# Kernel tuning notes

Hardware: AMD Instinct MI355X
Metric: run time of the kernel (lower is better)

The kernel has to match this reference:

```python
import jax, jax.numpy as jnp
import numpy as np

THRESH = 0.2  # contact probability threshold from _make_graph default


def setup_inputs() -> dict:
    key = jax.random.key(0)
    ks = jax.random.split(key, 10)
    L, D, K, M = 1024, 640, 32, 64
    S = jax.random.normal(ks[0], (L, D), jnp.float32)
    P = jax.random.uniform(ks[1], (L, L), jnp.float32)
    P = 0.5 * (P + P.T)  # symmetric base-pair probability matrix
    xyz = jax.random.normal(ks[2], (L, 3), jnp.float32) * 10.0  # Angstrom-scale C1' coords
    rbf_mu = jnp.linspace(0.0, 30.0, K).astype(jnp.float32)     # RBF centers over 0-30 A
    rbf_sigma = jax.random.uniform(ks[3], (K,), jnp.float32, 0.5, 2.0)
    W_edge = jax.random.normal(ks[4], (K + 2, M), jnp.float32) * 0.05
    b_edge = jnp.zeros((M,), jnp.float32)
    W_node = jax.random.normal(ks[5], (D, M), jnp.float32) * 0.05
    w_out = jax.random.normal(ks[6], (M,), jnp.float32) * 0.1
    return {"S": S, "P": P, "xyz": xyz, "rbf_mu": rbf_mu, "rbf_sigma": rbf_sigma,
            "W_edge": W_edge, "b_edge": b_edge, "W_node": W_node, "w_out": w_out}


def reference(S, P, xyz, rbf_mu, rbf_sigma, W_edge, b_edge, W_node, w_out):
    """Graph construction (_make_graph) + one SE3-style gated coordinate update.

    Edges: backbone (j == i+1, etype=0, pij=1) and high-prob contacts
    (P[i,j] > THRESH, j > i+2, etype=1, pij=P[i,j]). Edge scalars are
    [etype, pij, rbf(d)] exactly as in _make_graph; edge vectors are
    xyz[j]-xyz[i]. Computed in dense masked form for jit-compatibility.
    """
    L = xyz.shape[0]
    rel = xyz[None, :, :] - xyz[:, None, :]                      # (L,L,3) xyz[j]-xyz[i]
    # safe norm: eps avoids nan grad on zero diagonal (diagonal is masked out anyway)
    d = jnp.sqrt(jnp.sum(rel * rel, axis=-1, keepdims=True) + 1e-12)  # (L,L,1)
    rbf_feat = jnp.exp(-(d - rbf_mu) ** 2 / (2.0 * rbf_sigma ** 2))   # (L,L,K)

    idx = jnp.arange(L)
    backbone = idx[None, :] == idx[:, None] + 1                  # j == i+1
    contact = (P > THRESH) & (idx[None, :] > idx[:, None] + 2)   # skip j <= i+2
    mask = backbone | contact                                    # (L,L)

    etype = contact.astype(S.dtype)                              # 0 backbone, 1 contact
    pij = jnp.where(backbone, jnp.asarray(1.0, S.dtype), P)
    e_scalar = jnp.concatenate([etype[..., None], pij[..., None], rbf_feat], axis=-1)  # (L,L,K+2)

    # gather-compute: message from edge scalars + destination-node scalars
    node_proj = S @ W_node                                       # (L,M)
    msg = jax.nn.relu(jnp.einsum('ijk,km->ijm', e_scalar, W_edge) + b_edge
                      + node_proj[None, :, :])                   # (L,L,M)
    gate = jax.nn.sigmoid(msg @ w_out) * mask.astype(S.dtype)    # (L,L)

    # scatter: equivariant coordinate update, sum of gated edge vectors per node
    xyz_out = xyz + jnp.einsum('ij,ijc->ic', gate, rel)          # (L,3)
    return xyz_out
```

## Files before the change

### kernel.cpp

```cpp
#include <hip/hip_runtime.h>
#include <math.h>

#define LL 1024
#define DD 640
#define KK 32
#define MM 64
#define THRESH 0.2f
#define LOG2E 1.4426950408889634f

#define NPROJ_OFF  0
#define NPROJC_OFF (NPROJ_OFF + LL * MM)
#define WRT_OFF    (NPROJC_OFF + LL * MM)
#define W1_OFF     (WRT_OFF + 1024)
#define EA_OFF     (W1_OFF + MM)
#define EB_OFF     (EA_OFF + KK)
#define EC_OFF     (EB_OFF + KK)
#define XYZ4_OFF   (EC_OFF + KK)

typedef float f32x4_t __attribute__((ext_vector_type(4)));
typedef short bf16x8_t __attribute__((ext_vector_type(8)));

union FragU { unsigned int u[4]; bf16x8_t v; };

#if __has_builtin(__builtin_amdgcn_sqrtf)
#define FSQRT __builtin_amdgcn_sqrtf
#else
#define FSQRT sqrtf
#endif

#if __has_builtin(__builtin_amdgcn_exp2f)
#define EXP2F __builtin_amdgcn_exp2f
#else
#define EXP2F(x) __expf((x) * 0.6931471805599453f)
#endif

__device__ __forceinline__ unsigned int pack_bf(float hi, float lo) {
    return __builtin_amdgcn_perm(__float_as_uint(hi), __float_as_uint(lo), 0x07060302u);
}

__global__ __launch_bounds__(256) void prep_sk(
    const float* __restrict__ S, const float* __restrict__ xyz,
    const float* __restrict__ rbf_mu, const float* __restrict__ rbf_sigma,
    const float* __restrict__ W_edge, const float* __restrict__ b_edge,
    const float* __restrict__ W_node, float* __restrict__ ws)
{
    const int b = blockIdx.x;
    const int t = threadIdx.x;
    if (b < 256) {
        __shared__ float red[4][64][4];
        const int lane = t & 63;
        const int wave = t >> 6;
        const int r0   = (b >> 2) * 16;
        const int n0   = (b & 3) * 16;
        const int col  = lane & 15;
        const int quad = lane >> 4;

        f32x4_t acc = {0.f, 0.f, 0.f, 0.f};
        const float* arow = S + (size_t)(r0 + col) * DD + wave * 160 + quad * 8;
        const float* bcol = W_node + (size_t)(wave * 160 + quad * 8) * MM + n0 + col;

        #pragma unroll
        for (int ks = 0; ks < 5; ++ks) {
            const float4 a0 = *(const float4*)(arow + ks * 32);
            const float4 a1 = *(const float4*)(arow + ks * 32 + 4);
            FragU A;
            A.u[0] = pack_bf(a0.y, a0.x); A.u[1] = pack_bf(a0.w, a0.z);
            A.u[2] = pack_bf(a1.y, a1.x); A.u[3] = pack_bf(a1.w, a1.z);
            const float* bk = bcol + (size_t)ks * 32 * MM;
            const float b0 = bk[0 * MM], b1 = bk[1 * MM], b2 = bk[2 * MM], b3 = bk[3 * MM];
            const float b4 = bk[4 * MM], b5 = bk[5 * MM], b6 = bk[6 * MM], b7 = bk[7 * MM];
            FragU B;
            B.u[0] = pack_bf(b1, b0); B.u[1] = pack_bf(b3, b2);
            B.u[2] = pack_bf(b5, b4); B.u[3] = pack_bf(b7, b6);
            acc = __builtin_amdgcn_mfma_f32_16x16x32_bf16(A.v, B.v, acc, 0, 0, 0);
        }
        red[wave][lane][0] = acc[0];
        red[wave][lane][1] = acc[1];
        red[wave][lane][2] = acc[2];
        red[wave][lane][3] = acc[3];
        __syncthreads();
        const int lr  = t & 63;
        const int reg = t >> 6;
        const float v = (red[0][lr][reg] + red[1][lr][reg])
                      + (red[2][lr][reg] + red[3][lr][reg]);
        const int row = r0 + (lr >> 4) * 4 + reg;
        const int cc  = n0 + (lr & 15);
        const float vb = v + b_edge[cc];
        ws[NPROJ_OFF  + (size_t)row * MM + cc] = vb;
        ws[NPROJC_OFF + (size_t)row * MM + cc] = vb + W_edge[cc];
    } else {
        unsigned short* wrt = (unsigned short*)(ws + WRT_OFF);
        if (t < MM) ws[W1_OFF + t] = W_edge[MM + t];
        if (t < KK) {
            const float s  = rbf_sigma[t];
            const float m_ = rbf_mu[t];
            const float inv = 1.0f / (2.0f * s * s);
            ws[EA_OFF + t] = -LOG2E * inv;
            ws[EB_OFF + t] =  2.0f * LOG2E * inv * m_;
            ws[EC_OFF + t] = -LOG2E * inv * m_ * m_;
        }
        for (int idx = t; idx < KK * MM; idx += 256) {
            const int m = idx >> 5, k = idx & 31;
            unsigned int u = __float_as_uint(W_edge[(2 + k) * MM + m]);
            u = (u + 0x7fffu + ((u >> 16) & 1u)) >> 16;
            wrt[idx] = (unsigned short)u;
        }
        for (int n = t; n < LL; n += 256) {
            float4 v;
            v.x = xyz[3 * n + 0]; v.y = xyz[3 * n + 1];
            v.z = xyz[3 * n + 2]; v.w = 0.0f;
            *(float4*)(ws + XYZ4_OFF + 4 * n) = v;
        }
    }
}

__global__ __launch_bounds__(256) void edge_kernel3(
    const float* __restrict__ P, const float* __restrict__ w_out,
    const float* __restrict__ ws, float* __restrict__ out)
{
    const int tid  = threadIdx.x;
    const int lane = tid & 63;
    const int wave = tid >> 6;
    const int quad = lane >> 4;
    const int col  = lane & 15;
    __shared__ float sred[4][3];

    const float* __restrict__ nproj  = ws + NPROJ_OFF;
    const float* __restrict__ nprojc = ws + NPROJC_OFF;
    const float4* __restrict__ xyz4  = (const float4*)(ws + XYZ4_OFF);
    const unsigned short* __restrict__ wrt = (const unsigned short*)(ws + WRT_OFF);

    FragU ar[4];
    float w1r[16], wvr[16];
    float aj[8], bj[8], cj[8];
    #pragma unroll
    for (int mt = 0; mt < 4; ++mt) {
        const uint4 w = *(const uint4*)(wrt + (mt * 16 + col) * KK + quad * 8);
        ar[mt].u[0] = w.x; ar[mt].u[1] = w.y; ar[mt].u[2] = w.z; ar[mt].u[3] = w.w;
        const f32x4_t w1 = *(const f32x4_t*)(ws + W1_OFF + mt * 16 + quad * 4);
        const f32x4_t wo = *(const f32x4_t*)(w_out + mt * 16 + quad * 4);
        #pragma unroll
        for (int r = 0; r < 4; ++r) { w1r[mt * 4 + r] = w1[r]; wvr[mt * 4 + r] = wo[r]; }
    }
    #pragma unroll
    for (int j = 0; j < 8; ++j) {
        aj[j] = ws[EA_OFF + quad * 8 + j];
        bj[j] = ws[EB_OFF + quad * 8 + j];
        cj[j] = ws[EC_OFF + quad * 8 + j];
    }

    const int i = (int)blockIdx.x;
    const float4 xo = xyz4[i];
    const float xi0 = xo.x, xi1 = xo.y, xi2 = xo.z;
    const int len = (LL - 1) - i;
    float ax = 0.f, ay = 0.f, az = 0.f;
    const float* __restrict__ prow = P + (size_t)i * LL;

    for (int base = wave * 64; base < len; base += 256) {
        float pcv[4], dnv[4], q2v[4], dxv[4], dyv[4], dzv[4];
        const float* npr[4];
        float peff[4];
        #pragma unroll
        for (int ct = 0; ct < 4; ++ct) {
            const int jo_n = base + ct * 16 + col;
            int jc = i + 1 + jo_n;
            jc = (jc < LL) ? jc : (LL - 1);
            pcv[ct] = prow[jc];
            const float4 xn = xyz4[jc];
            dxv[ct] = xn.x - xi0; dyv[ct] = xn.y - xi1; dzv[ct] = xn.z - xi2;
            q2v[ct] = fmaf(dxv[ct], dxv[ct],
                      fmaf(dyv[ct], dyv[ct],
                      fmaf(dzv[ct], dzv[ct], 1e-12f)));
            dnv[ct] = FSQRT(q2v[ct]);
            const bool bb = (jo_n == 0);
            peff[ct] = bb ? 1.0f : pcv[ct];
            npr[ct] = (bb ? nproj : nprojc) + (size_t)jc * MM;
        }

        const int jo = base + lane;
        const bool valid = jo < len;
        float rx = dxv[0], ry = dyv[0], rz = dzv[0], p_own = pcv[0];
        rx = (quad == 1) ? dxv[1] : rx; rx = (quad == 2) ? dxv[2] : rx; rx = (quad == 3) ? dxv[3] : rx;
        ry = (quad == 1) ? dyv[1] : ry; ry = (quad == 2) ? dyv[2] : ry; ry = (quad == 3) ? dyv[3] : ry;
        rz = (quad == 1) ? dzv[1] : rz; rz = (quad == 2) ? dzv[2] : rz; rz = (quad == 3) ? dzv[3] : rz;
        p_own = (quad == 1) ? pcv[1] : p_own;
        p_own = (quad == 2) ? pcv[2] : p_own;
        p_own = (quad == 3) ? pcv[3] : p_own;
        const bool msk = valid && ((jo == 0) || ((jo >= 2) && (p_own > THRESH)));

        float e[4][8];
        #pragma unroll
        for (int ct = 0; ct < 4; ++ct)
            #pragma unroll
            for (int j = 0; j < 8; ++j)
                e[ct][j] = EXP2F(fmaf(aj[j], q2v[ct], fmaf(bj[j], dnv[ct], cj[j])));

        FragU bf[4];
        #pragma unroll
        for (int ct = 0; ct < 4; ++ct) {
            bf[ct].u[0] = pack_bf(e[ct][1], e[ct][0]);
            bf[ct].u[1] = pack_bf(e[ct][3], e[ct][2]);
            bf[ct].u[2] = pack_bf(e[ct][5], e[ct][4]);
            bf[ct].u[3] = pack_bf(e[ct][7], e[ct][6]);
        }

        float g[4] = {0.f, 0.f, 0.f, 0.f};
        #pragma unroll
        for (int mt = 0; mt < 4; ++mt) {
            f32x4_t c[4];
            #pragma unroll
            for (int ct = 0; ct < 4; ++ct)
                c[ct] = *(const f32x4_t*)(npr[ct] + mt * 16 + quad * 4);
            #pragma unroll
            for (int ct = 0; ct < 4; ++ct) {
                c[ct][0] = fmaf(peff[ct], w1r[mt*4+0], c[ct][0]);
                c[ct][1] = fmaf(peff[ct], w1r[mt*4+1], c[ct][1]);
                c[ct][2] = fmaf(peff[ct], w1r[mt*4+2], c[ct][2]);
                c[ct][3] = fmaf(peff[ct], w1r[mt*4+3], c[ct][3]);
            }
            #pragma unroll
            for (int ct = 0; ct < 4; ++ct)
                c[ct] = __builtin_amdgcn_mfma_f32_16x16x32_bf16(ar[mt].v, bf[ct].v, c[ct], 0, 0, 0);
            #pragma unroll
            for (int ct = 0; ct < 4; ++ct) {
                g[ct] = fmaf(fmaxf(c[ct][0], 0.f), wvr[mt*4+0], g[ct]);
                g[ct] = fmaf(fmaxf(c[ct][1], 0.f), wvr[mt*4+1], g[ct]);
                g[ct] = fmaf(fmaxf(c[ct][2], 0.f), wvr[mt*4+2], g[ct]);
                g[ct] = fmaf(fmaxf(c[ct][3], 0.f), wvr[mt*4+3], g[ct]);
            }
        }

        #pragma unroll
        for (int ct = 0; ct < 4; ++ct) g[ct] += __shfl_xor(g[ct], 16, 64);
        #pragma unroll
        for (int ct = 0; ct < 4; ++ct) g[ct] += __shfl_xor(g[ct], 32, 64);

        float gd = g[0];
        gd = (quad == 1) ? g[1] : gd;
        gd = (quad == 2) ? g[2] : gd;
        gd = (quad == 3) ? g[3] : gd;
        const float gate = msk ? (1.0f / (1.0f + __expf(-gd))) : 0.0f;
        ax = fmaf(gate, rx, ax);
        ay = fmaf(gate, ry, ay);
        az = fmaf(gate, rz, az);
    }

    #pragma unroll
    for (int off = 32; off > 0; off >>= 1) {
        ax += __shfl_down(ax, off, 64);
        ay += __shfl_down(ay, off, 64);
        az += __shfl_down(az, off, 64);
    }
    if (lane == 0) { sred[wave][0] = ax; sred[wave][1] = ay; sred[wave][2] = az; }
    __syncthreads();
    if (tid == 0) {
        const float tx = (sred[0][0] + sred[1][0]) + (sred[2][0] + sred[3][0]);
        const float ty = (sred[0][1] + sred[1][1]) + (sred[2][1] + sred[3][1]);
        const float tz = (sred[0][2] + sred[1][2]) + (sred[2][2] + sred[3][2]);
        out[i * 3 + 0] = xi0 + tx;
        out[i * 3 + 1] = xi1 + ty;
        out[i * 3 + 2] = xi2 + tz;
    }
}

extern "C" void kernel_launch(void* const* d_in, const int* in_sizes, int n_in,
                              void* d_out, int out_size, void* d_ws, size_t ws_size,
                              hipStream_t stream) {
    const float* S         = (const float*)d_in[0];
    const float* P         = (const float*)d_in[1];
    const float* xyz       = (const float*)d_in[2];
    const float* rbf_mu    = (const float*)d_in[3];
    const float* rbf_sigma = (const float*)d_in[4];
    const float* W_edge    = (const float*)d_in[5];
    const float* b_edge    = (const float*)d_in[6];
    const float* W_node    = (const float*)d_in[7];
    const float* w_out     = (const float*)d_in[8];
    float* out = (float*)d_out;
    float* ws  = (float*)d_ws;

    prep_sk<<<257, 256, 0, stream>>>(S, xyz, rbf_mu, rbf_sigma,
                                     W_edge, b_edge, W_node, ws);
    edge_kernel3<<<LL, 256, 0, stream>>>(P, w_out, ws, out);
}
```

Baseline: 97.50 us.

## Balance triangular edge work across blocks and shrink per-wave register footprint

Each block now handles the first half of row b and the second half of row L-1-b, so every block processes roughly equal numbers of edges instead of a triangular workload. Partial sums are combined with atomicAdd into an output pre-initialized with xyz by the prep kernel. The MFMA inner loop is restructured to process one column tile at a time, reducing live registers, and launch bounds request 4 blocks per SM for higher occupancy. Risks include less MFMA interleaving per tile, atomic overhead, and nondeterministic float summation order.

```diff
diff --git a/kernel.cpp b/kernel.cpp
--- a/kernel.cpp
+++ b/kernel.cpp
@@ -42,7 +42,8 @@
     const float* __restrict__ S, const float* __restrict__ xyz,
     const float* __restrict__ rbf_mu, const float* __restrict__ rbf_sigma,
     const float* __restrict__ W_edge, const float* __restrict__ b_edge,
-    const float* __restrict__ W_node, float* __restrict__ ws)
+    const float* __restrict__ W_node, float* __restrict__ ws,
+    float* __restrict__ out)
 {
     const int b = blockIdx.x;
     const int t = threadIdx.x;
@@ -111,10 +112,11 @@
             v.z = xyz[3 * n + 2]; v.w = 0.0f;
             *(float4*)(ws + XYZ4_OFF + 4 * n) = v;
         }
-    }
-}
-
-__global__ __launch_bounds__(256) void edge_kernel3(
+        for (int idx = t; idx < 3 * LL; idx += 256) out[idx] = xyz[idx];
+    }
+}
+
+__global__ __launch_bounds__(256, 4) void edge_kernel5(
     const float* __restrict__ P, const float* __restrict__ w_out,
     const float* __restrict__ ws, float* __restrict__ out)
 {
@@ -149,117 +151,102 @@
         cj[j] = ws[EC_OFF + quad * 8 + j];
     }
 
-    const int i = (int)blockIdx.x;
-    const float4 xo = xyz4[i];
-    const float xi0 = xo.x, xi1 = xo.y, xi2 = xo.z;
-    const int len = (LL - 1) - i;
-    float ax = 0.f, ay = 0.f, az = 0.f;
-    const float* __restrict__ prow = P + (size_t)i * LL;
-
-    for (int base = wave * 64; base < len; base += 256) {
-        float pcv[4], dnv[4], q2v[4], dxv[4], dyv[4], dzv[4];
-        const float* npr[4];
-        float peff[4];
-        #pragma unroll
-        for (int ct = 0; ct < 4; ++ct) {
-            const int jo_n = base + ct * 16 + col;
-            int jc = i + 1 + jo_n;
-            jc = (jc < LL) ? jc : (LL - 1);
-            pcv[ct] = prow[jc];
-            const float4 xn = xyz4[jc];
-            dxv[ct] = xn.x - xi0; dyv[ct] = xn.y - xi1; dzv[ct] = xn.z - xi2;
-            q2v[ct] = fmaf(dxv[ct], dxv[ct],
-                      fmaf(dyv[ct], dyv[ct],
-                      fmaf(dzv[ct], dzv[ct], 1e-12f)));
-            dnv[ct] = FSQRT(q2v[ct]);
-            const bool bb = (jo_n == 0);
-            peff[ct] = bb ? 1.0f : pcv[ct];
-            npr[ct] = (bb ? nproj : nprojc) + (size_t)jc * MM;
-        }
-
-        const int jo = base + lane;
-        const bool valid = jo < len;
-        float rx = dxv[0], ry = dyv[0], rz = dzv[0], p_own = pcv[0];
-        rx = (quad == 1) ? dxv[1] : rx; rx = (quad == 2) ? dxv[2] : rx; rx = (quad == 3) ? dxv[3] : rx;
-        ry = (quad == 1) ? dyv[1] : ry; ry = (quad == 2) ? dyv[2] : ry; ry = (quad == 3) ? dyv[3] : ry;
-        rz = (quad == 1) ? dzv[1] : rz; rz = (quad == 2) ? dzv[2] : rz; rz = (quad == 3) ? dzv[3] : rz;
-        p_own = (quad == 1) ? pcv[1] : p_own;
-        p_own = (quad == 2) ? pcv[2] : p_own;
-        p_own = (quad == 3) ? pcv[3] : p_own;
-        const bool msk = valid && ((jo == 0) || ((jo >= 2) && (p_own > THRESH)));
-
-        float e[4][8];
-        #pragma unroll
-        for (int ct = 0; ct < 4; ++ct)
-            #pragma unroll
-            for (int j = 0; j < 8; ++j)
-                e[ct][j] = EXP2F(fmaf(aj[j], q2v[ct], fmaf(bj[j], dnv[ct], cj[j])));
-
-        FragU bf[4];
-        #pragma unroll
-        for (int ct = 0; ct < 4; ++ct) {
-            bf[ct].u[0] = pack_bf(e[ct][1], e[ct][0]);
-            bf[ct].u[1] = pack_bf(e[ct][3], e[ct][2]);
-            bf[ct].u[2] = pack_bf(e[ct][5], e[ct][4]);
-            bf[ct].u[3] = pack_bf(e[ct][7], e[ct][6]);
-        }
-
-        float g[4] = {0.f, 0.f, 0.f, 0.f};
-        #pragma unroll
-        for (int mt = 0; mt < 4; ++mt) {
-            f32x4_t c[4];
-            #pragma unroll
-            for (int ct = 0; ct < 4; ++ct)
-                c[ct] = *(const f32x4_t*)(npr[ct] + mt * 16 + quad * 4);
+    const int b = (int)blockIdx.x;
+
+    #pragma unroll 1
+    for (int ss = 0; ss < 2; ++ss) {
+        int i, s0, s1;
+        if (ss == 0) {
+            i = b;
+            const int len = (LL - 1) - b;
+            s0 = 0; s1 = (len + 1) >> 1;
+        } else {
+            i = (LL - 1) - b;
+            const int len = b;
+            s0 = (len + 1) >> 1; s1 = len;
+        }
+        const float4 xo = xyz4[i];
+        const float xi0 = xo.x, xi1 = xo.y, xi2 = xo.z;
+        float ax = 0.f, ay = 0.f, az = 0.f;
+        const float* __restrict__ prow = P + (size_t)i * LL;
+
+        for (int base = s0 + wave * 64; base < s1; base += 256) {
+            const int jo = base + lane;
+            const bool valid = jo < s1;
+            const int jc_o = valid ? (i + 1 + jo) : (LL - 1);
+            const float p_own = prow[jc_o];
+            const float4 xj = xyz4[jc_o];
+            const float rx = xj.x - xi0, ry = xj.y - xi1, rz = xj.z - xi2;
+            const bool msk = valid && ((jo == 0) || ((jo >= 2) && (p_own > THRESH)));
+
+            float res[4];
             #pragma unroll
             for (int ct = 0; ct < 4; ++ct) {
-                c[ct][0] = fmaf(peff[ct], w1r[mt*4+0], c[ct][0]);
-                c[ct][1] = fmaf(peff[ct], w1r[mt*4+1], c[ct][1]);
-                c[ct][2] = fmaf(peff[ct], w1r[mt*4+2], c[ct][2]);
-                c[ct][3] = fmaf(peff[ct], w1r[mt*4+3], c[ct][3]);
+                const int jo_n = base + ct * 16 + col;
+                int jc = i + 1 + jo_n;
+                jc = (jc < LL) ? jc : (LL - 1);
+                const float p_n = prow[jc];
+                const float4 xn = xyz4[jc];
+                const float dx = xn.x - xi0, dy = xn.y - xi1, dz = xn.z - xi2;
+                const float q2 = fmaf(dx, dx, fmaf(dy, dy, fmaf(dz, dz, 1e-12f)));
+                const float d_n = FSQRT(q2);
+                const bool bb = (jo_n == 0);
+                const float peff = bb ? 1.0f : p_n;
+                const float* npr = (bb ? nproj : nprojc) + (size_t)jc * MM;
+
+                float e[8];
+                #pragma unroll
+                for (int j = 0; j < 8; ++j)
+                    e[j] = EXP2F(fmaf(aj[j], q2, fmaf(bj[j], d_n, cj[j])));
+                FragU bf;
+                bf.u[0] = pack_bf(e[1], e[0]); bf.u[1] = pack_bf(e[3], e[2]);
+                bf.u[2] = pack_bf(e[5], e[4]); bf.u[3] = pack_bf(e[7], e[6]);
+
+                float g = 0.0f;
+                #pragma unroll
+                for (int mt = 0; mt < 4; ++mt) {
+                    f32x4_t c0 = *(const f32x4_t*)(npr + mt * 16 + quad * 4);
+                    c0[0] = fmaf(peff, w1r[mt*4+0], c0[0]);
+                    c0[1] = fmaf(peff, w1r[mt*4+1], c0[1]);
+                    c0[2] = fmaf(peff, w1r[mt*4+2], c0[2]);
+                    c0[3] = fmaf(peff, w1r[mt*4+3], c0[3]);
+                    c0 = __builtin_amdgcn_mfma_f32_16x16x32_bf16(ar[mt].v, bf.v, c0, 0, 0, 0);
+                    g = fmaf(fmaxf(c0[0], 0.f), wvr[mt*4+0], g);
+                    g = fmaf(fmaxf(c0[1], 0.f), wvr[mt*4+1], g);
+                    g = fmaf(fmaxf(c0[2], 0.f), wvr[mt*4+2], g);
+                    g = fmaf(fmaxf(c0[3], 0.f), wvr[mt*4+3], g);
+                }
+                g += __shfl_xor(g, 16, 64);
+                g += __shfl_xor(g, 32, 64);
+                res[ct] = g;
             }
-            #pragma unroll
-            for (int ct = 0; ct < 4; ++ct)
-                c[ct] = __builtin_amdgcn_mfma_f32_16x16x32_bf16(ar[mt].v, bf[ct].v, c[ct], 0, 0, 0);
-            #pragma unroll
-            for (int ct = 0; ct < 4; ++ct) {
-                g[ct] = fmaf(fmaxf(c[ct][0], 0.f), wvr[mt*4+0], g[ct]);
-                g[ct] = fmaf(fmaxf(c[ct][1], 0.f), wvr[mt*4+1], g[ct]);
-                g[ct] = fmaf(fmaxf(c[ct][2], 0.f), wvr[mt*4+2], g[ct]);
-                g[ct] = fmaf(fmaxf(c[ct][3], 0.f), wvr[mt*4+3], g[ct]);
-            }
+            float gd = res[0];
+            gd = (quad == 1) ? res[1] : gd;
+            gd = (quad == 2) ? res[2] : gd;
+            gd = (quad == 3) ? res[3] : gd;
+            const float gate = msk ? (1.0f / (1.0f + __expf(-gd))) : 0.0f;
+            ax = fmaf(gate, rx, ax);
+            ay = fmaf(gate, ry, ay);
+            az = fmaf(gate, rz, az);
         }
 
         #pragma unroll
-        for (int ct = 0; ct < 4; ++ct) g[ct] += __shfl_xor(g[ct], 16, 64);
-        #pragma unroll
-        for (int ct = 0; ct < 4; ++ct) g[ct] += __shfl_xor(g[ct], 32, 64);
-
-        float gd = g[0];
-        gd = (quad == 1) ? g[1] : gd;
-        gd = (quad == 2) ? g[2] : gd;
-        gd = (quad == 3) ? g[3] : gd;
-        const float gate = msk ? (1.0f / (1.0f + __expf(-gd))) : 0.0f;
-        ax = fmaf(gate, rx, ax);
-        ay = fmaf(gate, ry, ay);
-        az = fmaf(gate, rz, az);
-    }
-
-    #pragma unroll
-    for (int off = 32; off > 0; off >>= 1) {
-        ax += __shfl_down(ax, off, 64);
-        ay += __shfl_down(ay, off, 64);
-        az += __shfl_down(az, off, 64);
-    }
-    if (lane == 0) { sred[wave][0] = ax; sred[wave][1] = ay; sred[wave][2] = az; }
-    __syncthreads();
-    if (tid == 0) {
-        const float tx = (sred[0][0] + sred[1][0]) + (sred[2][0] + sred[3][0]);
-        const float ty = (sred[0][1] + sred[1][1]) + (sred[2][1] + sred[3][1]);
-        const float tz = (sred[0][2] + sred[1][2]) + (sred[2][2] + sred[3][2]);
-        out[i * 3 + 0] = xi0 + tx;
-        out[i * 3 + 1] = xi1 + ty;
-        out[i * 3 + 2] = xi2 + tz;
+        for (int off = 32; off > 0; off >>= 1) {
+            ax += __shfl_down(ax, off, 64);
+            ay += __shfl_down(ay, off, 64);
+            az += __shfl_down(az, off, 64);
+        }
+        if (lane == 0) { sred[wave][0] = ax; sred[wave][1] = ay; sred[wave][2] = az; }
+        __syncthreads();
+        if (tid == 0) {
+            const float tx = (sred[0][0] + sred[1][0]) + (sred[2][0] + sred[3][0]);
+            const float ty = (sred[0][1] + sred[1][1]) + (sred[2][1] + sred[3][1]);
+            const float tz = (sred[0][2] + sred[1][2]) + (sred[2][2] + sred[3][2]);
+            atomicAdd(out + i * 3 + 0, tx);
+            atomicAdd(out + i * 3 + 1, ty);
+            atomicAdd(out + i * 3 + 2, tz);
+        }
+        __syncthreads();
     }
 }
 
@@ -279,6 +266,6 @@
     float* ws  = (float*)d_ws;
 
     prep_sk<<<257, 256, 0, stream>>>(S, xyz, rbf_mu, rbf_sigma,
-                                     W_edge, b_edge, W_node, ws);
-    edge_kernel3<<<LL, 256, 0, stream>>>(P, w_out, ws, out);
-}
+                                     W_edge, b_edge, W_node, ws, out);
+    edge_kernel5<<<LL, 256, 0, stream>>>(P, w_out, ws, out);
+}
```

Result: slower. 101.1 us (+3.7%).
